# Kernel tuning notes

Measured on AMD Instinct MI355X. Metric: run time of the kernel, lower is better.

Reference implementation:

```python
import jax, jax.numpy as jnp
import numpy as np

N_EXPERTS = 20
DIM = 32
EPS = 1e-12  # F.normalize eps


def setup_inputs() -> dict:
    key = jax.random.key(0)
    k_x, k_pos, k_w1, k_b1, k_w0, k_b0 = jax.random.split(key, 6)
    B = 131072
    bound = 1.0 / np.sqrt(DIM)  # torch Linear default init range
    return {
        "x": jax.random.normal(k_x, (B, DIM), dtype=jnp.float32),
        "W1": jax.random.uniform(k_w1, (N_EXPERTS, DIM, DIM), jnp.float32, -bound, bound),
        "b1": jax.random.uniform(k_b1, (N_EXPERTS, DIM), jnp.float32, -bound, bound),
        "W0": jax.random.uniform(k_w0, (N_EXPERTS, DIM, DIM), jnp.float32, -bound, bound),
        "b0": jax.random.uniform(k_b0, (N_EXPERTS, DIM), jnp.float32, -bound, bound),
        "pos": jax.random.randint(k_pos, (B,), 0, N_EXPERTS, dtype=jnp.int64),
    }


def reference(x, W1, b1, W0, b0, pos):
    # Gather per-sample expert weights (routing): [B, DIM, DIM] / [B, DIM]
    W1g, b1g = W1[pos], b1[pos]
    W0g, b0g = W0[pos], b0[pos]
    # fc1: y = x @ W1^T + b1 (torch Linear convention, W is [out, in])
    h = jnp.einsum("bi,boi->bo", x, W1g) + b1g
    # fc0
    out = jnp.einsum("bi,boi->bo", h, W0g) + b0g
    # F.normalize(dim=-1): x / max(||x||_2, eps)
    norm = jnp.sqrt(jnp.sum(out * out, axis=-1, keepdims=True))
    return out / jnp.maximum(norm, EPS)
```

## Files before the change

kernel.cpp:

```cpp
#include <hip/hip_runtime.h>
#include <stdint.h>

#define N_EXPERTS 20
#define DIM 32
#define SPB 256
#define MAIN_T 256
#define MROW 40
#define MAX_TILES 48

using frag_ab = __attribute__((ext_vector_type(8))) short;
using frag_cd = __attribute__((ext_vector_type(4))) float;

static __device__ __forceinline__ short f2bf(float f) {
    union { float f; uint32_t u; } v; v.f = f;
    uint32_t u = v.u;
    return (short)(uint16_t)((u + 0x7FFFu + ((u >> 16) & 1u)) >> 16);
}

__global__ __launch_bounds__(256) void k_prep(
    const float* __restrict__ W1, const float* __restrict__ b1,
    const float* __restrict__ W0, const float* __restrict__ b0,
    unsigned short* __restrict__ Mbf, float* __restrict__ cvec)
{
    __shared__ float s1[1024], s0[1024];
    int e = blockIdx.x, t = threadIdx.x;
    const float* w1 = W1 + e * 1024;
    const float* w0 = W0 + e * 1024;
    for (int i = t; i < 1024; i += 256) { s1[i] = w1[i]; s0[i] = w0[i]; }
    __syncthreads();
    for (int idx = t; idx < 1024; idx += 256) {
        int o = idx >> 5, i = idx & 31;
        float s = 0.f;
        #pragma unroll
        for (int k = 0; k < 32; k++) s += s0[o*32 + k] * s1[k*32 + i];
        Mbf[e*1024 + o*32 + i] = (unsigned short)f2bf(s);
    }
    if (t < DIM) {
        float s = b0[e*32 + t];
        #pragma unroll
        for (int k = 0; k < 32; k++) s += s0[t*32 + k] * b1[e*32 + k];
        cvec[e*32 + t] = s;
    }
}

__global__ __launch_bounds__(MAIN_T) void k_moe(
    const float* __restrict__ x, const int* __restrict__ pos,
    const unsigned short* __restrict__ Mbf, const float* __restrict__ cvec,
    float* __restrict__ out, int B)
{
    __shared__ unsigned short Ms[N_EXPERTS * 32 * MROW];
    __shared__ float cs[N_EXPERTS * 32];
    __shared__ int hist[N_EXPERTS];
    __shared__ int lstart[N_EXPERTS + 1];
    __shared__ int cursor[N_EXPERTS];
    __shared__ int lidx[SPB];
    __shared__ int tileE[MAX_TILES], tileB[MAX_TILES];
    __shared__ int ntiles;

    int t = threadIdx.x;
    int base = blockIdx.x * SPB;
    int S = min(SPB, B - base);
    if (S <= 0) return;

    if (t < N_EXPERTS) hist[t] = 0;
    __syncthreads();

    {
        const uint32_t* msrc = (const uint32_t*)Mbf;
        uint32_t* mdst = (uint32_t*)Ms;
        for (int d = t; d < N_EXPERTS * 512; d += MAIN_T) {
            int e = d >> 9, rem = d & 511;
            int n = rem >> 4, c = rem & 15;
            mdst[e * (32 * MROW / 2) + n * (MROW / 2) + c] = msrc[d];
        }
        for (int i = t; i < N_EXPERTS * 32; i += MAIN_T) cs[i] = cvec[i];
    }
    int my_e = -1;
    if (t < S) {
        my_e = pos[base + t];
        atomicAdd(&hist[my_e], 1);
    }
    __syncthreads();

    int lane = t & 63, wave = t >> 6;

    if (wave == 0) {
        int e = lane;
        int h = (e < N_EXPERTS) ? hist[e] : 0;
        int s = h;
        #pragma unroll
        for (int d = 1; d < 32; d <<= 1) { int v = __shfl_up(s, d); if (lane >= d) s += v; }
        int pre = s - h;
        int ntl = (h + 15) >> 4;
        int ts = ntl;
        #pragma unroll
        for (int d = 1; d < 32; d <<= 1) { int v = __shfl_up(ts, d); if (lane >= d) ts += v; }
        int tpre = ts - ntl;
        if (e < N_EXPERTS) {
            lstart[e] = pre; cursor[e] = pre;
            for (int k = 0; k < ntl; k++) { tileE[tpre + k] = e; tileB[tpre + k] = pre + 16 * k; }
            if (e == N_EXPERTS - 1) { lstart[N_EXPERTS] = pre + h; ntiles = tpre + ntl; }
        }
    }
    __syncthreads();

    if (t < S) {
        int slot = atomicAdd(&cursor[my_e], 1);
        lidx[slot] = t;
    }
    __syncthreads();

    int nt = ntiles;
    int n = lane & 15, q = lane >> 4;

    int ti = wave;
    float4 xa, xb;
    int cur_e = 0, cur_tb = 0, cur_bend = 0;
    if (ti < nt) {
        cur_e = tileE[ti]; cur_tb = tileB[ti]; cur_bend = lstart[cur_e + 1];
        int slot = min(cur_tb + n, cur_bend - 1);
        int l = lidx[slot];
        const float* xr = x + (size_t)(base + l) * 32 + q * 8;
        xa = *(const float4*)xr; xb = *(const float4*)(xr + 4);
    }
    for (; ti < nt; ti += 4) {
        int e = cur_e, tb = cur_tb, bend = cur_bend;
        float4 a0 = xa, a1 = xb;
        int tj = ti + 4;
        if (tj < nt) {
            cur_e = tileE[tj]; cur_tb = tileB[tj]; cur_bend = lstart[cur_e + 1];
            int slot = min(cur_tb + n, cur_bend - 1);
            int l = lidx[slot];
            const float* xr = x + (size_t)(base + l) * 32 + q * 8;
            xa = *(const float4*)xr; xb = *(const float4*)(xr + 4);
        }

        const unsigned short* mrow = Ms + e * 32 * MROW;
        frag_ab bf0 = *(const frag_ab*)(mrow + n * MROW + q * 8);
        frag_ab bf1 = *(const frag_ab*)(mrow + (n + 16) * MROW + q * 8);
        float c0 = cs[e * 32 + n];
        float c1 = cs[e * 32 + 16 + n];

        frag_ab af;
        af[0] = f2bf(a0.x); af[1] = f2bf(a0.y); af[2] = f2bf(a0.z); af[3] = f2bf(a0.w);
        af[4] = f2bf(a1.x); af[5] = f2bf(a1.y); af[6] = f2bf(a1.z); af[7] = f2bf(a1.w);

        frag_cd z = {0.f, 0.f, 0.f, 0.f};
        frag_cd d0 = __builtin_amdgcn_mfma_f32_16x16x32_bf16(af, bf0, z, 0, 0, 0);
        frag_cd d1 = __builtin_amdgcn_mfma_f32_16x16x32_bf16(af, bf1, z, 0, 0, 0);

        #pragma unroll
        for (int r = 0; r < 4; r++) {
            int os = tb + q * 4 + r;
            float v0 = d0[r] + c0;
            float v1 = d1[r] + c1;
            float ss = v0 * v0 + v1 * v1;
            ss += __shfl_xor(ss, 1);
            ss += __shfl_xor(ss, 2);
            ss += __shfl_xor(ss, 4);
            ss += __shfl_xor(ss, 8);
            float sc = rsqrtf(fmaxf(ss, 1e-24f));
            if (os < bend) {
                int lo = lidx[os];
                float* op = out + (size_t)(base + lo) * 32;
                op[n]      = v0 * sc;
                op[16 + n] = v1 * sc;
            }
        }
    }
}

extern "C" void kernel_launch(void* const* d_in, const int* in_sizes, int n_in,
                              void* d_out, int out_size, void* d_ws, size_t ws_size,
                              hipStream_t stream) {
    const float* x  = (const float*)d_in[0];
    const float* W1 = (const float*)d_in[1];
    const float* b1 = (const float*)d_in[2];
    const float* W0 = (const float*)d_in[3];
    const float* b0 = (const float*)d_in[4];
    const int*  pos = (const int*)d_in[5];
    float* out = (float*)d_out;
    int B = in_sizes[0] / DIM;

    char* ws = (char*)d_ws;
    unsigned short* Mbf = (unsigned short*)ws;
    float* cvec = (float*)(ws + (size_t)N_EXPERTS * 1024 * 2);

    k_prep<<<N_EXPERTS, 256, 0, stream>>>(W1, b1, W0, b0, Mbf, cvec);
    int nblk = (B + SPB - 1) / SPB;
    k_moe<<<nblk, MAIN_T, 0, stream>>>(x, pos, Mbf, cvec, out, B);
}
```

Before: 89.62 us.

## Stage x tile into LDS as bf16 with coalesced loads, use 512 threads

The x rows for the block are now loaded contiguously and coalesced by all threads, converted to bf16 and stored in an LDS buffer, instead of each wave gathering scattered rows from global memory inside the tile loop with software prefetch. The block size doubles to 512 threads (8 waves) with a min-blocks hint, and the pos load is issued before the first barrier so it overlaps the histogram reset. This removes the uncoalesced global gather latency from the MFMA loop, at the cost of extra LDS (about 20KB), another staging pass, and possible occupancy limits from the larger shared footprint.

```diff
diff --git a/kernel.cpp b/kernel.cpp
--- a/kernel.cpp
+++ b/kernel.cpp
@@ -4,8 +4,9 @@
 #define N_EXPERTS 20
 #define DIM 32
 #define SPB 256
-#define MAIN_T 256
+#define MAIN_T 512
 #define MROW 40
+#define XROW 40
 #define MAX_TILES 48
 
 using frag_ab = __attribute__((ext_vector_type(8))) short;
@@ -43,12 +44,13 @@
     }
 }
 
-__global__ __launch_bounds__(MAIN_T) void k_moe(
+__global__ __launch_bounds__(MAIN_T, 4) void k_moe(
     const float* __restrict__ x, const int* __restrict__ pos,
     const unsigned short* __restrict__ Mbf, const float* __restrict__ cvec,
     float* __restrict__ out, int B)
 {
     __shared__ unsigned short Ms[N_EXPERTS * 32 * MROW];
+    __shared__ unsigned short Xs[SPB * XROW];
     __shared__ float cs[N_EXPERTS * 32];
     __shared__ int hist[N_EXPERTS];
     __shared__ int lstart[N_EXPERTS + 1];
@@ -63,7 +65,10 @@
     if (S <= 0) return;
 
     if (t < N_EXPERTS) hist[t] = 0;
+    int my_e = -1;
+    if (t < S) my_e = pos[base + t];
     __syncthreads();
+    if (t < S) atomicAdd(&hist[my_e], 1);
 
     {
         const uint32_t* msrc = (const uint32_t*)Mbf;
@@ -75,10 +80,21 @@
         }
         for (int i = t; i < N_EXPERTS * 32; i += MAIN_T) cs[i] = cvec[i];
     }
-    int my_e = -1;
-    if (t < S) {
-        my_e = pos[base + t];
-        atomicAdd(&hist[my_e], 1);
+    for (int d = t; d < 2 * S; d += MAIN_T) {
+        int s = d >> 1, half = d & 1;
+        const float* xr = x + (size_t)(base + s) * 32 + half * 16;
+        float4 a = *(const float4*)(xr);
+        float4 b = *(const float4*)(xr + 4);
+        float4 c = *(const float4*)(xr + 8);
+        float4 e4 = *(const float4*)(xr + 12);
+        frag_ab v0, v1;
+        v0[0] = f2bf(a.x); v0[1] = f2bf(a.y); v0[2] = f2bf(a.z); v0[3] = f2bf(a.w);
+        v0[4] = f2bf(b.x); v0[5] = f2bf(b.y); v0[6] = f2bf(b.z); v0[7] = f2bf(b.w);
+        v1[0] = f2bf(c.x); v1[1] = f2bf(c.y); v1[2] = f2bf(c.z); v1[3] = f2bf(c.w);
+        v1[4] = f2bf(e4.x); v1[5] = f2bf(e4.y); v1[6] = f2bf(e4.z); v1[7] = f2bf(e4.w);
+        unsigned short* xd = (unsigned short*)Xs + s * XROW + half * 16;
+        *(frag_ab*)(xd)     = v0;
+        *(frag_ab*)(xd + 8) = v1;
     }
     __syncthreads();
 
@@ -113,37 +129,20 @@
     int nt = ntiles;
     int n = lane & 15, q = lane >> 4;
 
-    int ti = wave;
-    float4 xa, xb;
-    int cur_e = 0, cur_tb = 0, cur_bend = 0;
-    if (ti < nt) {
-        cur_e = tileE[ti]; cur_tb = tileB[ti]; cur_bend = lstart[cur_e + 1];
-        int slot = min(cur_tb + n, cur_bend - 1);
+    for (int ti = wave; ti < nt; ti += (MAIN_T / 64)) {
+        int e = tileE[ti], tb = tileB[ti];
+        int bend = lstart[e + 1];
+
+        int slot = min(tb + n, bend - 1);
         int l = lidx[slot];
-        const float* xr = x + (size_t)(base + l) * 32 + q * 8;
-        xa = *(const float4*)xr; xb = *(const float4*)(xr + 4);
-    }
-    for (; ti < nt; ti += 4) {
-        int e = cur_e, tb = cur_tb, bend = cur_bend;
-        float4 a0 = xa, a1 = xb;
-        int tj = ti + 4;
-        if (tj < nt) {
-            cur_e = tileE[tj]; cur_tb = tileB[tj]; cur_bend = lstart[cur_e + 1];
-            int slot = min(cur_tb + n, cur_bend - 1);
-            int l = lidx[slot];
-            const float* xr = x + (size_t)(base + l) * 32 + q * 8;
-            xa = *(const float4*)xr; xb = *(const float4*)(xr + 4);
-        }
+
+        frag_ab af = *(const frag_ab*)((const unsigned short*)Xs + l * XROW + q * 8);
 
         const unsigned short* mrow = Ms + e * 32 * MROW;
         frag_ab bf0 = *(const frag_ab*)(mrow + n * MROW + q * 8);
         frag_ab bf1 = *(const frag_ab*)(mrow + (n + 16) * MROW + q * 8);
         float c0 = cs[e * 32 + n];
         float c1 = cs[e * 32 + 16 + n];
-
-        frag_ab af;
-        af[0] = f2bf(a0.x); af[1] = f2bf(a0.y); af[2] = f2bf(a0.z); af[3] = f2bf(a0.w);
-        af[4] = f2bf(a1.x); af[5] = f2bf(a1.y); af[6] = f2bf(a1.z); af[7] = f2bf(a1.w);
 
         frag_cd z = {0.f, 0.f, 0.f, 0.f};
         frag_cd d0 = __builtin_amdgcn_mfma_f32_16x16x32_bf16(af, bf0, z, 0, 0, 0);
```

Result: faster. 86.78 us (-3.2%).
